# Kernel tuning notes

Hardware: AMD Instinct MI355X
Metric: run time of the kernel (lower is better)

The kernel has to match this reference:

```python
import jax, jax.numpy as jnp
import numpy as np

N_NODES = 200000
N_EDGES = 6400000
N_LAYERS = 3
Z_DIM = 4  # 2*4 + 1 + 3 == 12 == Linear in_features


def setup_inputs() -> dict:
    key = jax.random.key(0)
    ks = jax.random.split(key, 7)
    z = jax.random.normal(ks[0], (N_NODES, Z_DIM), dtype=jnp.float32)
    r = jax.random.uniform(ks[1], (N_EDGES, 1), dtype=jnp.float32)
    r_hat = jax.random.normal(ks[2], (N_EDGES, 3), dtype=jnp.float32)
    # Per-layer Linear(12, 1) weights and biases, stacked over layers.
    W = jax.random.normal(ks[3], (N_LAYERS, 1, 12), dtype=jnp.float32) * (1.0 / np.sqrt(12.0))
    b = jnp.zeros((N_LAYERS, 1), dtype=jnp.float32)
    src = jax.random.randint(ks[4], (N_EDGES,), 0, N_NODES, dtype=jnp.int32)
    dst = jax.random.randint(ks[5], (N_EDGES,), 0, N_NODES, dtype=jnp.int32)
    return {"z": z, "r": r, "r_hat": r_hat, "W": W, "b": b, "src": src, "dst": dst}


def reference(z, r, r_hat, W, b, src, dst):
    # batch['x'] = batch['z'].copy()
    x = z
    n_nodes = z.shape[0]
    for i in range(W.shape[0]):
        # Per-edge gather + concat -> [E, 12]
        inpt = jnp.concatenate([z[src], z[dst], r, r_hat], axis=-1)
        # Tiny Linear(12, 1) -> per-edge scalar message [E, 1]
        msg = inpt @ W[i].T + b[i]
        # Scatter-sum messages onto destination nodes, residual update.
        agg = jax.ops.segment_sum(msg, dst, num_segments=n_nodes)  # [N, 1]
        z = z + agg  # broadcast over the 4 node features
    return z, x
```

## Files before the change

kernel.cpp:

```cpp
#include <hip/hip_runtime.h>

#define N_NODES 200000
#define N_EDGES 6400000
#define K_BUCKETS 256
#define BUCKET 784
#define NSB 3200
#define CHUNK 2000
#define P_SPLIT 8

__device__ __forceinline__ unsigned short f2bf(float x) {
    unsigned u = __float_as_uint(x);
    u += 0x7fffu + ((u >> 16) & 1u);
    return (unsigned short)(u >> 16);
}
__device__ __forceinline__ float bf2f(unsigned short h) {
    return __uint_as_float((unsigned)h << 16);
}


__global__ __launch_bounds__(256) void prep_kernel(
    const float4* __restrict__ z, float4* __restrict__ x_out,
    const float* __restrict__ W,
    float* __restrict__ u, float* __restrict__ v)
{
    int n = blockIdx.x * 256 + threadIdx.x;
    if (n >= N_NODES) return;
    float4 zv = z[n];
    x_out[n] = zv;
    float a0 = W[0], a1 = W[1], a2 = W[2], a3 = W[3];
    float q0 = W[4], q1 = W[5], q2 = W[6], q3 = W[7];
    u[n] = a0 * zv.x + a1 * zv.y + a2 * zv.z + a3 * zv.w;
    v[n] = q0 * zv.x + q1 * zv.y + q2 * zv.z + q3 * zv.w;
}

__global__ __launch_bounds__(256) void hist_kernel(const int* __restrict__ dst,
                                                   int* __restrict__ counts)
{
    __shared__ int cnt[K_BUCKETS];
    int tid = threadIdx.x, sb = blockIdx.x;
    cnt[tid] = 0;
    __syncthreads();
    int e0 = sb * CHUNK;
    for (int i = tid; i < CHUNK; i += 256)
        atomicAdd(&cnt[dst[e0 + i] / BUCKET], 1);
    __syncthreads();
    counts[sb * K_BUCKETS + tid] = cnt[tid];
}

__global__ __launch_bounds__(256) void scan_cols(const int* __restrict__ counts,
                                                 int* __restrict__ baseRel,
                                                 int* __restrict__ tot)
{
    __shared__ int buf[256];
    __shared__ int carry_s;
    int k = blockIdx.x, tid = threadIdx.x;
    if (tid == 0) carry_s = 0;
    __syncthreads();
    for (int base = 0; base < NSB; base += 256) {
        int idx = base + tid;
        int v = (idx < NSB) ? counts[idx * K_BUCKETS + k] : 0;
        buf[tid] = v;
        __syncthreads();
        for (int off = 1; off < 256; off <<= 1) {
            int t = (tid >= off) ? buf[tid - off] : 0;
            __syncthreads();
            buf[tid] += t;
            __syncthreads();
        }
        int incl = buf[tid];
        if (idx < NSB) baseRel[idx * K_BUCKETS + k] = carry_s + incl - v;
        __syncthreads();
        if (tid == 255) carry_s += incl;
        __syncthreads();
    }
    if (tid == 255) tot[k] = carry_s;
}

__global__ __launch_bounds__(256) void scan_tot(const int* __restrict__ tot,
                                                int* __restrict__ bstart)
{
    __shared__ int buf[256];
    int tid = threadIdx.x;
    int v = tot[tid];
    buf[tid] = v;
    __syncthreads();
    for (int off = 1; off < 256; off <<= 1) {
        int t = (tid >= off) ? buf[tid - off] : 0;
        __syncthreads();
        buf[tid] += t;
        __syncthreads();
    }
    bstart[tid] = buf[tid] - v;
    if (tid == 255) bstart[256] = buf[255];
}

__global__ __launch_bounds__(256) void scatter_kernel(
    const int* __restrict__ src, const int* __restrict__ dst,
    const float* __restrict__ r, const float* __restrict__ r_hat,
    const float* __restrict__ W, const float* __restrict__ b,
    const int* __restrict__ counts, const int* __restrict__ baseRel,
    const int* __restrict__ bstart,
    int* __restrict__ packedA, unsigned* __restrict__ c01a,
    unsigned short* __restrict__ c2a)
{
    __shared__ int cur[K_BUCKETS];
    __shared__ int delta[K_BUCKETS];
    __shared__ int scanbuf[256];
    __shared__ int            lpack[CHUNK];
    __shared__ unsigned       lc01[CHUNK];
    __shared__ unsigned short lc2[CHUNK];
    __shared__ unsigned char  skb[CHUNK];

    int tid = threadIdx.x, sb = blockIdx.x;

    int v = counts[sb * K_BUCKETS + tid];
    scanbuf[tid] = v;
    __syncthreads();
    for (int off = 1; off < 256; off <<= 1) {
        int t = (tid >= off) ? scanbuf[tid - off] : 0;
        __syncthreads();
        scanbuf[tid] += t;
        __syncthreads();
    }
    int localBase = scanbuf[tid] - v;
    int gBase = bstart[tid] + baseRel[sb * K_BUCKETS + tid];
    delta[tid] = gBase - localBase;
    cur[tid] = localBase;
    __syncthreads();

    float w8_0 = W[8],  w9_0 = W[9],  w10_0 = W[10], w11_0 = W[11], b0 = b[0];
    float w8_1 = W[20], w9_1 = W[21], w10_1 = W[22], w11_1 = W[23], b1 = b[1];
    float w8_2 = W[32], w9_2 = W[33], w10_2 = W[34], w11_2 = W[35], b2 = b[2];

    int e0 = sb * CHUNK;
    for (int i = tid; i < CHUNK; i += 256) {
        int e = e0 + i;
        int d = dst[e];
        int k = d / BUCKET;
        int dl = d - k * BUCKET;
        int slot = atomicAdd(&cur[k], 1);
        int sn = src[e];
        float rv = r[e];
        size_t he = 3 * (size_t)e;
        float h0 = r_hat[he], h1 = r_hat[he + 1], h2 = r_hat[he + 2];
        lpack[slot] = (sn << 10) | dl;
        unsigned cc0 = f2bf(w8_0 * rv + w9_0 * h0 + w10_0 * h1 + w11_0 * h2 + b0);
        unsigned cc1 = f2bf(w8_1 * rv + w9_1 * h0 + w10_1 * h1 + w11_1 * h2 + b1);
        lc01[slot] = cc0 | (cc1 << 16);
        lc2[slot]  = f2bf(w8_2 * rv + w9_2 * h0 + w10_2 * h1 + w11_2 * h2 + b2);
        skb[slot]  = (unsigned char)k;
    }
    __syncthreads();

    for (int s = tid; s < CHUNK; s += 256) {
        int k = skb[s];
        int gpos = delta[k] + s;
        packedA[gpos] = lpack[s];
        c01a[gpos] = lc01[s];
        c2a[gpos]  = lc2[s];
    }
}

__global__ __launch_bounds__(256) void pagg_kernel(
    const int* __restrict__ packedA, const unsigned* __restrict__ c01a,
    const unsigned short* __restrict__ c2a, const int* __restrict__ bstart,
    const float* __restrict__ u, const float* __restrict__ v,
    int layer, float* __restrict__ partial)
{
    __shared__ float vsl[BUCKET];
    __shared__ float aggsl[BUCKET];
    int tid = threadIdx.x, blk = blockIdx.x;
    int k = blk / P_SPLIT;
    int p = blk - k * P_SPLIT;
    int nbase = k * BUCKET;
    int nn = min(BUCKET, N_NODES - nbase);

    for (int i = tid; i < BUCKET; i += 256) {
        aggsl[i] = 0.0f;
        vsl[i] = (i < nn) ? v[nbase + i] : 0.0f;
    }
    __syncthreads();

    int estart = bstart[k], eend = bstart[k + 1];
    int len = eend - estart;
    int per = (len + P_SPLIT - 1) / P_SPLIT;
    int lo = estart + p * per;
    int hi = min(lo + per, eend);

    for (int j = lo + tid; j < hi; j += 256) {
        int pack = packedA[j];
        int s = pack >> 10;
        int dl = pack & 1023;
        float c = (layer == 2) ? bf2f(c2a[j])
                               : bf2f((unsigned short)(c01a[j] >> (16 * layer)));
        atomicAdd(&aggsl[dl], u[s] + vsl[dl] + c);
    }
    __syncthreads();

    float* pout = partial + (size_t)blk * BUCKET;
    for (int i = tid; i < BUCKET; i += 256) pout[i] = aggsl[i];
}

__global__ __launch_bounds__(256) void fin_kernel(
    const float4* __restrict__ z0, const float* __restrict__ partial,
    const float* __restrict__ Sin, float* __restrict__ Sout,
    const float* __restrict__ W, int layer,
    float* __restrict__ u, float* __restrict__ v, float4* __restrict__ z_out)
{
    int n = blockIdx.x * 256 + threadIdx.x;
    if (n >= N_NODES) return;
    int k = n / BUCKET;
    int i = n - k * BUCKET;
    float agg = 0.0f;
    const float* pk = partial + (size_t)k * P_SPLIT * BUCKET + i;
#pragma unroll
    for (int p = 0; p < P_SPLIT; ++p) agg += pk[(size_t)p * BUCKET];
    float S = ((layer == 0) ? 0.0f : Sin[n]) + agg;
    if (layer < 2) {
        const float* Wn = W + 12 * (layer + 1);
        float a0 = Wn[0], a1 = Wn[1], a2 = Wn[2], a3 = Wn[3];
        float q0 = Wn[4], q1 = Wn[5], q2 = Wn[6], q3 = Wn[7];
        float A = a0 + a1 + a2 + a3, B = q0 + q1 + q2 + q3;
        float4 zv = z0[n];
        Sout[n] = S;
        u[n] = a0 * zv.x + a1 * zv.y + a2 * zv.z + a3 * zv.w + A * S;
        v[n] = q0 * zv.x + q1 * zv.y + q2 * zv.z + q3 * zv.w + B * S;
    } else {
        float4 zv = z0[n];
        zv.x += S; zv.y += S; zv.z += S; zv.w += S;
        z_out[n] = zv;
    }
}


__global__ __launch_bounds__(256) void init_kernel(
    const float4* __restrict__ z_in, float4* __restrict__ z_cur,
    float4* __restrict__ x_out, float* __restrict__ agg)
{
    int n = blockIdx.x * blockDim.x + threadIdx.x;
    if (n < N_NODES) {
        float4 vv = z_in[n];
        z_cur[n] = vv; x_out[n] = vv; agg[n] = 0.0f;
    }
}

__global__ __launch_bounds__(256) void edge_kernel(
    const float* __restrict__ z, const float* __restrict__ r,
    const float* __restrict__ r_hat, const int* __restrict__ src,
    const int* __restrict__ dst, const float* __restrict__ Wl,
    const float* __restrict__ bl, float* __restrict__ agg)
{
    int e = blockIdx.x * blockDim.x + threadIdx.x;
    if (e >= N_EDGES) return;
    float w0 = Wl[0], w1 = Wl[1], w2 = Wl[2], w3 = Wl[3];
    float w4 = Wl[4], w5 = Wl[5], w6 = Wl[6], w7 = Wl[7];
    float w8 = Wl[8], w9 = Wl[9], w10 = Wl[10], w11 = Wl[11];
    float bias = bl[0];
    int s = src[e], d = dst[e];
    float4 zs = ((const float4*)z)[s];
    float4 zd = ((const float4*)z)[d];
    float rv = r[e];
    const float* rh = r_hat + 3 * (size_t)e;
    float msg = w0*zs.x + w1*zs.y + w2*zs.z + w3*zs.w
              + w4*zd.x + w5*zd.y + w6*zd.z + w7*zd.w
              + w8*rv + w9*rh[0] + w10*rh[1] + w11*rh[2] + bias;
    unsafeAtomicAdd(&agg[d], msg);
}

__global__ __launch_bounds__(256) void node_update(float4* __restrict__ z_cur,
                                                   float* __restrict__ agg)
{
    int n = blockIdx.x * blockDim.x + threadIdx.x;
    if (n < N_NODES) {
        float a = agg[n]; float4 vv = z_cur[n];
        vv.x += a; vv.y += a; vv.z += a; vv.w += a;
        z_cur[n] = vv; agg[n] = 0.0f;
    }
}

__global__ __launch_bounds__(256) void final_update(const float4* __restrict__ z_cur,
                                                    const float* __restrict__ agg,
                                                    float4* __restrict__ z_out)
{
    int n = blockIdx.x * blockDim.x + threadIdx.x;
    if (n < N_NODES) {
        float a = agg[n]; float4 vv = z_cur[n];
        vv.x += a; vv.y += a; vv.z += a; vv.w += a;
        z_out[n] = vv;
    }
}


extern "C" void kernel_launch(void* const* d_in, const int* in_sizes, int n_in,
                              void* d_out, int out_size, void* d_ws, size_t ws_size,
                              hipStream_t stream)
{
    const float* z     = (const float*)d_in[0];
    const float* r     = (const float*)d_in[1];
    const float* r_hat = (const float*)d_in[2];
    const float* W     = (const float*)d_in[3];
    const float* b     = (const float*)d_in[4];
    const int*   src   = (const int*)d_in[5];
    const int*   dst   = (const int*)d_in[6];
    float* out = (float*)d_out;

    char* ws = (char*)d_ws;
    size_t off = 0;
    auto alloc = [&](size_t bytes) {
        void* p = ws + off;
        off += (bytes + 15) & ~(size_t)15;
        return p;
    };
    int*            packedA = (int*)alloc((size_t)N_EDGES * 4);
    unsigned*       c01a    = (unsigned*)alloc((size_t)N_EDGES * 4);
    unsigned short* c2a     = (unsigned short*)alloc((size_t)N_EDGES * 2);
    int*            counts  = (int*)alloc((size_t)NSB * K_BUCKETS * 4);
    int*            baseRel = (int*)alloc((size_t)NSB * K_BUCKETS * 4);
    int*            tot     = (int*)alloc((size_t)K_BUCKETS * 4);
    int*            bstart  = (int*)alloc((size_t)(K_BUCKETS + 1) * 4);
    float*          Sa      = (float*)alloc((size_t)N_NODES * 4);
    float*          Sb      = (float*)alloc((size_t)N_NODES * 4);
    float*          ubuf    = (float*)alloc((size_t)N_NODES * 4);
    float*          vbuf    = (float*)alloc((size_t)N_NODES * 4);
    float*          partial = (float*)alloc((size_t)K_BUCKETS * P_SPLIT * BUCKET * 4);
    size_t required = off;

    dim3 nblk((N_NODES + 255) / 256);

    if (ws_size >= required) {
        prep_kernel<<<nblk, 256, 0, stream>>>(
            (const float4*)z, (float4*)(out + 4 * (size_t)N_NODES), W, ubuf, vbuf);
        hist_kernel<<<NSB, 256, 0, stream>>>(dst, counts);
        scan_cols<<<K_BUCKETS, 256, 0, stream>>>(counts, baseRel, tot);
        scan_tot<<<1, 256, 0, stream>>>(tot, bstart);
        scatter_kernel<<<NSB, 256, 0, stream>>>(src, dst, r, r_hat, W, b,
                                                counts, baseRel, bstart,
                                                packedA, c01a, c2a);
        pagg_kernel<<<K_BUCKETS * P_SPLIT, 256, 0, stream>>>(
            packedA, c01a, c2a, bstart, ubuf, vbuf, 0, partial);
        fin_kernel<<<nblk, 256, 0, stream>>>(
            (const float4*)z, partial, Sa, Sa, W, 0, ubuf, vbuf, (float4*)out);
        pagg_kernel<<<K_BUCKETS * P_SPLIT, 256, 0, stream>>>(
            packedA, c01a, c2a, bstart, ubuf, vbuf, 1, partial);
        fin_kernel<<<nblk, 256, 0, stream>>>(
            (const float4*)z, partial, Sa, Sb, W, 1, ubuf, vbuf, (float4*)out);
        pagg_kernel<<<K_BUCKETS * P_SPLIT, 256, 0, stream>>>(
            packedA, c01a, c2a, bstart, ubuf, vbuf, 2, partial);
        fin_kernel<<<nblk, 256, 0, stream>>>(
            (const float4*)z, partial, Sb, Sb, W, 2, ubuf, vbuf, (float4*)out);
    } else {
        float* agg   = (float*)d_ws;
        float* z_cur = agg + N_NODES;
        dim3 eblk((N_EDGES + 255) / 256);
        init_kernel<<<nblk, 256, 0, stream>>>(
            (const float4*)z, (float4*)z_cur,
            (float4*)(out + 4 * (size_t)N_NODES), agg);
        for (int i = 0; i < 3; ++i) {
            edge_kernel<<<eblk, 256, 0, stream>>>(
                z_cur, r, r_hat, src, dst, W + 12 * i, b + i, agg);
            if (i < 2)
                node_update<<<nblk, 256, 0, stream>>>((float4*)z_cur, agg);
            else
                final_update<<<nblk, 256, 0, stream>>>(
                    (const float4*)z_cur, agg, (float4*)out);
        }
    }
}
```

Before: 403.5 us.

## Precompute all-layer z-dependent edge sums in one pass, then run lean SpMV layers

The per-layer edge aggregation is split algebraically. One fused pass over the sorted edges gathers bf16-packed initial node features and accumulates, for all three layers at once, the initial-feature message sums plus in-degree. The two remaining layers then need only a plain SpMV of the running residual S over the edges. This cuts per-edge reads of u, v and the constant arrays in later layers, in exchange for four shared atomics per edge in the first pass, larger float4 partial buffers, and bf16 rounding of z.

```diff
diff --git a/kernel.cpp b/kernel.cpp
--- a/kernel.cpp
+++ b/kernel.cpp
@@ -20,17 +20,15 @@
 
 __global__ __launch_bounds__(256) void prep_kernel(
     const float4* __restrict__ z, float4* __restrict__ x_out,
-    const float* __restrict__ W,
-    float* __restrict__ u, float* __restrict__ v)
+    ushort4* __restrict__ zb)
 {
     int n = blockIdx.x * 256 + threadIdx.x;
     if (n >= N_NODES) return;
     float4 zv = z[n];
     x_out[n] = zv;
-    float a0 = W[0], a1 = W[1], a2 = W[2], a3 = W[3];
-    float q0 = W[4], q1 = W[5], q2 = W[6], q3 = W[7];
-    u[n] = a0 * zv.x + a1 * zv.y + a2 * zv.z + a3 * zv.w;
-    v[n] = q0 * zv.x + q1 * zv.y + q2 * zv.z + q3 * zv.w;
+    ushort4 q;
+    q.x = f2bf(zv.x); q.y = f2bf(zv.y); q.z = f2bf(zv.z); q.w = f2bf(zv.w);
+    zb[n] = q;
 }
 
 __global__ __launch_bounds__(256) void hist_kernel(const int* __restrict__ dst,
@@ -161,25 +159,25 @@
     }
 }
 
-__global__ __launch_bounds__(256) void pagg_kernel(
+__global__ __launch_bounds__(256) void ypass_kernel(
     const int* __restrict__ packedA, const unsigned* __restrict__ c01a,
     const unsigned short* __restrict__ c2a, const int* __restrict__ bstart,
-    const float* __restrict__ u, const float* __restrict__ v,
-    int layer, float* __restrict__ partial)
-{
-    __shared__ float vsl[BUCKET];
-    __shared__ float aggsl[BUCKET];
+    const ushort4* __restrict__ zb, const float* __restrict__ W,
+    float4* __restrict__ gpart)
+{
+    __shared__ float g0sl[BUCKET], g1sl[BUCKET], g2sl[BUCKET], dgsl[BUCKET];
     int tid = threadIdx.x, blk = blockIdx.x;
     int k = blk / P_SPLIT;
     int p = blk - k * P_SPLIT;
-    int nbase = k * BUCKET;
-    int nn = min(BUCKET, N_NODES - nbase);
 
     for (int i = tid; i < BUCKET; i += 256) {
-        aggsl[i] = 0.0f;
-        vsl[i] = (i < nn) ? v[nbase + i] : 0.0f;
-    }
-    __syncthreads();
+        g0sl[i] = 0.f; g1sl[i] = 0.f; g2sl[i] = 0.f; dgsl[i] = 0.f;
+    }
+    __syncthreads();
+
+    float a00 = W[0],  a01 = W[1],  a02 = W[2],  a03 = W[3];
+    float a10 = W[12], a11 = W[13], a12 = W[14], a13 = W[15];
+    float a20 = W[24], a21 = W[25], a22 = W[26], a23 = W[27];
 
     int estart = bstart[k], eend = bstart[k + 1];
     int len = eend - estart;
@@ -191,44 +189,106 @@
         int pack = packedA[j];
         int s = pack >> 10;
         int dl = pack & 1023;
-        float c = (layer == 2) ? bf2f(c2a[j])
-                               : bf2f((unsigned short)(c01a[j] >> (16 * layer)));
-        atomicAdd(&aggsl[dl], u[s] + vsl[dl] + c);
-    }
-    __syncthreads();
-
-    float* pout = partial + (size_t)blk * BUCKET;
-    for (int i = tid; i < BUCKET; i += 256) pout[i] = aggsl[i];
-}
-
-__global__ __launch_bounds__(256) void fin_kernel(
-    const float4* __restrict__ z0, const float* __restrict__ partial,
-    const float* __restrict__ Sin, float* __restrict__ Sout,
-    const float* __restrict__ W, int layer,
-    float* __restrict__ u, float* __restrict__ v, float4* __restrict__ z_out)
+        ushort4 zq = zb[s];
+        float z0v = bf2f(zq.x), z1v = bf2f(zq.y), z2v = bf2f(zq.z), z3v = bf2f(zq.w);
+        unsigned cc = c01a[j];
+        float c0 = bf2f((unsigned short)(cc & 0xffff));
+        float c1 = bf2f((unsigned short)(cc >> 16));
+        float c2 = bf2f(c2a[j]);
+        atomicAdd(&g0sl[dl], a00*z0v + a01*z1v + a02*z2v + a03*z3v + c0);
+        atomicAdd(&g1sl[dl], a10*z0v + a11*z1v + a12*z2v + a13*z3v + c1);
+        atomicAdd(&g2sl[dl], a20*z0v + a21*z1v + a22*z2v + a23*z3v + c2);
+        atomicAdd(&dgsl[dl], 1.0f);
+    }
+    __syncthreads();
+
+    float4* pout = gpart + (size_t)blk * BUCKET;
+    for (int i = tid; i < BUCKET; i += 256) {
+        float4 o; o.x = g0sl[i]; o.y = g1sl[i]; o.z = g2sl[i]; o.w = dgsl[i];
+        pout[i] = o;
+    }
+}
+
+__global__ __launch_bounds__(256) void fin0_kernel(
+    const float4* __restrict__ gpart, const float4* __restrict__ z0,
+    const float* __restrict__ W,
+    float* __restrict__ g1, float* __restrict__ g2, float* __restrict__ deg,
+    float* __restrict__ S1)
 {
     int n = blockIdx.x * 256 + threadIdx.x;
     if (n >= N_NODES) return;
     int k = n / BUCKET;
     int i = n - k * BUCKET;
-    float agg = 0.0f;
+    const float4* pk = gpart + (size_t)k * P_SPLIT * BUCKET + i;
+    float4 acc = pk[0];
+#pragma unroll
+    for (int p = 1; p < P_SPLIT; ++p) {
+        float4 t = pk[(size_t)p * BUCKET];
+        acc.x += t.x; acc.y += t.y; acc.z += t.z; acc.w += t.w;
+    }
+    g1[n] = acc.y; g2[n] = acc.z; deg[n] = acc.w;
+    float q0 = W[4], q1 = W[5], q2 = W[6], q3 = W[7];
+    float4 zv = z0[n];
+    S1[n] = acc.x + acc.w * (q0*zv.x + q1*zv.y + q2*zv.z + q3*zv.w);
+}
+
+__global__ __launch_bounds__(256) void spmv_kernel(
+    const int* __restrict__ packedA, const int* __restrict__ bstart,
+    const float* __restrict__ S, float* __restrict__ partial)
+{
+    __shared__ float tsl[BUCKET];
+    int tid = threadIdx.x, blk = blockIdx.x;
+    int k = blk / P_SPLIT;
+    int p = blk - k * P_SPLIT;
+    for (int i = tid; i < BUCKET; i += 256) tsl[i] = 0.f;
+    __syncthreads();
+
+    int estart = bstart[k], eend = bstart[k + 1];
+    int len = eend - estart;
+    int per = (len + P_SPLIT - 1) / P_SPLIT;
+    int lo = estart + p * per;
+    int hi = min(lo + per, eend);
+
+    for (int j = lo + tid; j < hi; j += 256) {
+        int pack = packedA[j];
+        int s = pack >> 10;
+        int dl = pack & 1023;
+        atomicAdd(&tsl[dl], S[s]);
+    }
+    __syncthreads();
+    float* pout = partial + (size_t)blk * BUCKET;
+    for (int i = tid; i < BUCKET; i += 256) pout[i] = tsl[i];
+}
+
+template<int LAST>
+__global__ __launch_bounds__(256) void finl_kernel(
+    const float* __restrict__ partial, const float* __restrict__ gl,
+    const float* __restrict__ deg, const float4* __restrict__ z0,
+    const float* __restrict__ Sin, float* __restrict__ Sout,
+    const float* __restrict__ W, int layer, float4* __restrict__ z_out)
+{
+    int n = blockIdx.x * 256 + threadIdx.x;
+    if (n >= N_NODES) return;
+    int k = n / BUCKET;
+    int i = n - k * BUCKET;
     const float* pk = partial + (size_t)k * P_SPLIT * BUCKET + i;
+    float t = 0.f;
 #pragma unroll
-    for (int p = 0; p < P_SPLIT; ++p) agg += pk[(size_t)p * BUCKET];
-    float S = ((layer == 0) ? 0.0f : Sin[n]) + agg;
-    if (layer < 2) {
-        const float* Wn = W + 12 * (layer + 1);
-        float a0 = Wn[0], a1 = Wn[1], a2 = Wn[2], a3 = Wn[3];
-        float q0 = Wn[4], q1 = Wn[5], q2 = Wn[6], q3 = Wn[7];
-        float A = a0 + a1 + a2 + a3, B = q0 + q1 + q2 + q3;
-        float4 zv = z0[n];
-        Sout[n] = S;
-        u[n] = a0 * zv.x + a1 * zv.y + a2 * zv.z + a3 * zv.w + A * S;
-        v[n] = q0 * zv.x + q1 * zv.y + q2 * zv.z + q3 * zv.w + B * S;
+    for (int p = 0; p < P_SPLIT; ++p) t += pk[(size_t)p * BUCKET];
+    const float* Wl = W + 12 * layer;
+    float a0 = Wl[0], a1 = Wl[1], a2 = Wl[2], a3 = Wl[3];
+    float q0 = Wl[4], q1 = Wl[5], q2 = Wl[6], q3 = Wl[7];
+    float A = a0 + a1 + a2 + a3, B = q0 + q1 + q2 + q3;
+    float S = Sin[n];
+    float4 zv = z0[n];
+    float agg = gl[n] + A * t + deg[n] * (q0*zv.x + q1*zv.y + q2*zv.z + q3*zv.w + B * S);
+    float Sn = S + agg;
+    if (LAST) {
+        float4 o = zv;
+        o.x += Sn; o.y += Sn; o.z += Sn; o.w += Sn;
+        z_out[n] = o;
     } else {
-        float4 zv = z0[n];
-        zv.x += S; zv.y += S; zv.z += S; zv.w += S;
-        z_out[n] = zv;
+        Sout[n] = Sn;
     }
 }
 
@@ -318,36 +378,37 @@
     int*            baseRel = (int*)alloc((size_t)NSB * K_BUCKETS * 4);
     int*            tot     = (int*)alloc((size_t)K_BUCKETS * 4);
     int*            bstart  = (int*)alloc((size_t)(K_BUCKETS + 1) * 4);
+    ushort4*        zb      = (ushort4*)alloc((size_t)N_NODES * 8);
+    float4*         gpart   = (float4*)alloc((size_t)K_BUCKETS * P_SPLIT * BUCKET * 16);
+    float*          g1      = (float*)alloc((size_t)N_NODES * 4);
+    float*          g2      = (float*)alloc((size_t)N_NODES * 4);
+    float*          deg     = (float*)alloc((size_t)N_NODES * 4);
     float*          Sa      = (float*)alloc((size_t)N_NODES * 4);
     float*          Sb      = (float*)alloc((size_t)N_NODES * 4);
-    float*          ubuf    = (float*)alloc((size_t)N_NODES * 4);
-    float*          vbuf    = (float*)alloc((size_t)N_NODES * 4);
-    float*          partial = (float*)alloc((size_t)K_BUCKETS * P_SPLIT * BUCKET * 4);
+    float*          pspmv   = (float*)alloc((size_t)K_BUCKETS * P_SPLIT * BUCKET * 4);
     size_t required = off;
 
     dim3 nblk((N_NODES + 255) / 256);
 
     if (ws_size >= required) {
         prep_kernel<<<nblk, 256, 0, stream>>>(
-            (const float4*)z, (float4*)(out + 4 * (size_t)N_NODES), W, ubuf, vbuf);
+            (const float4*)z, (float4*)(out + 4 * (size_t)N_NODES), zb);
         hist_kernel<<<NSB, 256, 0, stream>>>(dst, counts);
         scan_cols<<<K_BUCKETS, 256, 0, stream>>>(counts, baseRel, tot);
         scan_tot<<<1, 256, 0, stream>>>(tot, bstart);
         scatter_kernel<<<NSB, 256, 0, stream>>>(src, dst, r, r_hat, W, b,
                                                 counts, baseRel, bstart,
                                                 packedA, c01a, c2a);
-        pagg_kernel<<<K_BUCKETS * P_SPLIT, 256, 0, stream>>>(
-            packedA, c01a, c2a, bstart, ubuf, vbuf, 0, partial);
-        fin_kernel<<<nblk, 256, 0, stream>>>(
-            (const float4*)z, partial, Sa, Sa, W, 0, ubuf, vbuf, (float4*)out);
-        pagg_kernel<<<K_BUCKETS * P_SPLIT, 256, 0, stream>>>(
-            packedA, c01a, c2a, bstart, ubuf, vbuf, 1, partial);
-        fin_kernel<<<nblk, 256, 0, stream>>>(
-            (const float4*)z, partial, Sa, Sb, W, 1, ubuf, vbuf, (float4*)out);
-        pagg_kernel<<<K_BUCKETS * P_SPLIT, 256, 0, stream>>>(
-            packedA, c01a, c2a, bstart, ubuf, vbuf, 2, partial);
-        fin_kernel<<<nblk, 256, 0, stream>>>(
-            (const float4*)z, partial, Sb, Sb, W, 2, ubuf, vbuf, (float4*)out);
+        ypass_kernel<<<K_BUCKETS * P_SPLIT, 256, 0, stream>>>(
+            packedA, c01a, c2a, bstart, zb, W, gpart);
+        fin0_kernel<<<nblk, 256, 0, stream>>>(
+            gpart, (const float4*)z, W, g1, g2, deg, Sa);
+        spmv_kernel<<<K_BUCKETS * P_SPLIT, 256, 0, stream>>>(packedA, bstart, Sa, pspmv);
+        finl_kernel<0><<<nblk, 256, 0, stream>>>(
+            pspmv, g1, deg, (const float4*)z, Sa, Sb, W, 1, (float4*)out);
+        spmv_kernel<<<K_BUCKETS * P_SPLIT, 256, 0, stream>>>(packedA, bstart, Sb, pspmv);
+        finl_kernel<1><<<nblk, 256, 0, stream>>>(
+            pspmv, g2, deg, (const float4*)z, Sb, Sa, W, 2, (float4*)out);
     } else {
         float* agg   = (float*)d_ws;
         float* z_cur = agg + N_NODES;
```

New measurement: 495.4 us. 22.8% more time.

## Factor destination term out of edge aggregation using in-degree and split bf16 coefficient arrays

Applied to the files above, without the earlier changes.

The per-edge dst-node term v[dst] is pulled out of the scatter loop and applied once per node as degree times v, with in-degree counted in the first aggregation pass. The edge pass now reads one gathered src-node table and one compact bf16 coefficient array per layer, where before it loaded a packed 32-bit pair. The aggregation, scatter and histogram loops are also unrolled, with int4 loads for dst, to raise memory-level parallelism. The trade-off is an extra shared-memory atomic and partial buffer in the first pass and a per-node degree array.

```diff
diff --git a/kernel.cpp b/kernel.cpp
--- a/kernel.cpp
+++ b/kernel.cpp
@@ -20,17 +20,13 @@
 
 __global__ __launch_bounds__(256) void prep_kernel(
     const float4* __restrict__ z, float4* __restrict__ x_out,
-    const float* __restrict__ W,
-    float* __restrict__ u, float* __restrict__ v)
+    const float* __restrict__ W, float* __restrict__ wtab)
 {
     int n = blockIdx.x * 256 + threadIdx.x;
     if (n >= N_NODES) return;
     float4 zv = z[n];
     x_out[n] = zv;
-    float a0 = W[0], a1 = W[1], a2 = W[2], a3 = W[3];
-    float q0 = W[4], q1 = W[5], q2 = W[6], q3 = W[7];
-    u[n] = a0 * zv.x + a1 * zv.y + a2 * zv.z + a3 * zv.w;
-    v[n] = q0 * zv.x + q1 * zv.y + q2 * zv.z + q3 * zv.w;
+    wtab[n] = W[0]*zv.x + W[1]*zv.y + W[2]*zv.z + W[3]*zv.w;
 }
 
 __global__ __launch_bounds__(256) void hist_kernel(const int* __restrict__ dst,
@@ -41,8 +37,14 @@
     cnt[tid] = 0;
     __syncthreads();
     int e0 = sb * CHUNK;
-    for (int i = tid; i < CHUNK; i += 256)
-        atomicAdd(&cnt[dst[e0 + i] / BUCKET], 1);
+    const int4* d4p = (const int4*)(dst + e0);
+    for (int i4 = tid; i4 < CHUNK / 4; i4 += 256) {
+        int4 d4 = d4p[i4];
+        atomicAdd(&cnt[d4.x / BUCKET], 1);
+        atomicAdd(&cnt[d4.y / BUCKET], 1);
+        atomicAdd(&cnt[d4.z / BUCKET], 1);
+        atomicAdd(&cnt[d4.w / BUCKET], 1);
+    }
     __syncthreads();
     counts[sb * K_BUCKETS + tid] = cnt[tid];
 }
@@ -100,14 +102,16 @@
     const float* __restrict__ W, const float* __restrict__ b,
     const int* __restrict__ counts, const int* __restrict__ baseRel,
     const int* __restrict__ bstart,
-    int* __restrict__ packedA, unsigned* __restrict__ c01a,
+    int* __restrict__ packedA,
+    unsigned short* __restrict__ c0a, unsigned short* __restrict__ c1a,
     unsigned short* __restrict__ c2a)
 {
     __shared__ int cur[K_BUCKETS];
     __shared__ int delta[K_BUCKETS];
     __shared__ int scanbuf[256];
     __shared__ int            lpack[CHUNK];
-    __shared__ unsigned       lc01[CHUNK];
+    __shared__ unsigned short lc0[CHUNK];
+    __shared__ unsigned short lc1[CHUNK];
     __shared__ unsigned short lc2[CHUNK];
     __shared__ unsigned char  skb[CHUNK];
 
@@ -133,7 +137,33 @@
     float w8_2 = W[32], w9_2 = W[33], w10_2 = W[34], w11_2 = W[35], b2 = b[2];
 
     int e0 = sb * CHUNK;
-    for (int i = tid; i < CHUNK; i += 256) {
+    int i = tid;
+    for (; i + 256 < CHUNK; i += 512) {
+        int ea = e0 + i, eb = e0 + i + 256;
+        int da = dst[ea], db = dst[eb];
+        int sa = src[ea], sb2 = src[eb];
+        float ra = r[ea], rb = r[eb];
+        size_t ha = 3 * (size_t)ea, hb = 3 * (size_t)eb;
+        float a0h = r_hat[ha], a1h = r_hat[ha+1], a2h = r_hat[ha+2];
+        float b0h = r_hat[hb], b1h = r_hat[hb+1], b2h = r_hat[hb+2];
+
+        int ka = da / BUCKET, dla = da - ka * BUCKET;
+        int slota = atomicAdd(&cur[ka], 1);
+        lpack[slota] = (sa << 10) | dla;
+        lc0[slota] = f2bf(w8_0*ra + w9_0*a0h + w10_0*a1h + w11_0*a2h + b0);
+        lc1[slota] = f2bf(w8_1*ra + w9_1*a0h + w10_1*a1h + w11_1*a2h + b1);
+        lc2[slota] = f2bf(w8_2*ra + w9_2*a0h + w10_2*a1h + w11_2*a2h + b2);
+        skb[slota] = (unsigned char)ka;
+
+        int kb = db / BUCKET, dlb = db - kb * BUCKET;
+        int slotb = atomicAdd(&cur[kb], 1);
+        lpack[slotb] = (sb2 << 10) | dlb;
+        lc0[slotb] = f2bf(w8_0*rb + w9_0*b0h + w10_0*b1h + w11_0*b2h + b0);
+        lc1[slotb] = f2bf(w8_1*rb + w9_1*b0h + w10_1*b1h + w11_1*b2h + b1);
+        lc2[slotb] = f2bf(w8_2*rb + w9_2*b0h + w10_2*b1h + w11_2*b2h + b2);
+        skb[slotb] = (unsigned char)kb;
+    }
+    for (; i < CHUNK; i += 256) {
         int e = e0 + i;
         int d = dst[e];
         int k = d / BUCKET;
@@ -142,13 +172,12 @@
         int sn = src[e];
         float rv = r[e];
         size_t he = 3 * (size_t)e;
-        float h0 = r_hat[he], h1 = r_hat[he + 1], h2 = r_hat[he + 2];
+        float h0 = r_hat[he], h1 = r_hat[he+1], h2 = r_hat[he+2];
         lpack[slot] = (sn << 10) | dl;
-        unsigned cc0 = f2bf(w8_0 * rv + w9_0 * h0 + w10_0 * h1 + w11_0 * h2 + b0);
-        unsigned cc1 = f2bf(w8_1 * rv + w9_1 * h0 + w10_1 * h1 + w11_1 * h2 + b1);
-        lc01[slot] = cc0 | (cc1 << 16);
-        lc2[slot]  = f2bf(w8_2 * rv + w9_2 * h0 + w10_2 * h1 + w11_2 * h2 + b2);
-        skb[slot]  = (unsigned char)k;
+        lc0[slot] = f2bf(w8_0*rv + w9_0*h0 + w10_0*h1 + w11_0*h2 + b0);
+        lc1[slot] = f2bf(w8_1*rv + w9_1*h0 + w10_1*h1 + w11_1*h2 + b1);
+        lc2[slot] = f2bf(w8_2*rv + w9_2*h0 + w10_2*h1 + w11_2*h2 + b2);
+        skb[slot] = (unsigned char)k;
     }
     __syncthreads();
 
@@ -156,28 +185,27 @@
         int k = skb[s];
         int gpos = delta[k] + s;
         packedA[gpos] = lpack[s];
-        c01a[gpos] = lc01[s];
-        c2a[gpos]  = lc2[s];
-    }
-}
-
-__global__ __launch_bounds__(256) void pagg_kernel(
-    const int* __restrict__ packedA, const unsigned* __restrict__ c01a,
-    const unsigned short* __restrict__ c2a, const int* __restrict__ bstart,
-    const float* __restrict__ u, const float* __restrict__ v,
-    int layer, float* __restrict__ partial)
-{
-    __shared__ float vsl[BUCKET];
-    __shared__ float aggsl[BUCKET];
+        c0a[gpos] = lc0[s];
+        c1a[gpos] = lc1[s];
+        c2a[gpos] = lc2[s];
+    }
+}
+
+template<int FIRST>
+__global__ __launch_bounds__(256) void gpass_kernel(
+    const int* __restrict__ packedA, const unsigned short* __restrict__ cb,
+    const int* __restrict__ bstart, const float* __restrict__ wtab,
+    float* __restrict__ gpart, float* __restrict__ dpart)
+{
+    __shared__ float gsl[BUCKET];
+    __shared__ float dsl[FIRST ? BUCKET : 1];
     int tid = threadIdx.x, blk = blockIdx.x;
     int k = blk / P_SPLIT;
     int p = blk - k * P_SPLIT;
-    int nbase = k * BUCKET;
-    int nn = min(BUCKET, N_NODES - nbase);
 
     for (int i = tid; i < BUCKET; i += 256) {
-        aggsl[i] = 0.0f;
-        vsl[i] = (i < nn) ? v[nbase + i] : 0.0f;
+        gsl[i] = 0.0f;
+        if (FIRST) dsl[i] = 0.0f;
     }
     __syncthreads();
 
@@ -187,48 +215,86 @@
     int lo = estart + p * per;
     int hi = min(lo + per, eend);
 
-    for (int j = lo + tid; j < hi; j += 256) {
-        int pack = packedA[j];
-        int s = pack >> 10;
-        int dl = pack & 1023;
-        float c = (layer == 2) ? bf2f(c2a[j])
-                               : bf2f((unsigned short)(c01a[j] >> (16 * layer)));
-        atomicAdd(&aggsl[dl], u[s] + vsl[dl] + c);
-    }
-    __syncthreads();
-
-    float* pout = partial + (size_t)blk * BUCKET;
-    for (int i = tid; i < BUCKET; i += 256) pout[i] = aggsl[i];
+    int j = lo + tid;
+    for (; j + 768 < hi; j += 1024) {
+        int p0 = packedA[j];
+        int p1 = packedA[j + 256];
+        int p2 = packedA[j + 512];
+        int p3 = packedA[j + 768];
+        unsigned short q0 = cb[j], q1 = cb[j + 256], q2 = cb[j + 512], q3 = cb[j + 768];
+        float g0 = wtab[p0 >> 10];
+        float g1 = wtab[p1 >> 10];
+        float g2 = wtab[p2 >> 10];
+        float g3 = wtab[p3 >> 10];
+        atomicAdd(&gsl[p0 & 1023], g0 + bf2f(q0));
+        atomicAdd(&gsl[p1 & 1023], g1 + bf2f(q1));
+        atomicAdd(&gsl[p2 & 1023], g2 + bf2f(q2));
+        atomicAdd(&gsl[p3 & 1023], g3 + bf2f(q3));
+        if (FIRST) {
+            atomicAdd(&dsl[p0 & 1023], 1.0f);
+            atomicAdd(&dsl[p1 & 1023], 1.0f);
+            atomicAdd(&dsl[p2 & 1023], 1.0f);
+            atomicAdd(&dsl[p3 & 1023], 1.0f);
+        }
+    }
+    for (; j < hi; j += 256) {
+        int pk = packedA[j];
+        atomicAdd(&gsl[pk & 1023], wtab[pk >> 10] + bf2f(cb[j]));
+        if (FIRST) atomicAdd(&dsl[pk & 1023], 1.0f);
+    }
+    __syncthreads();
+
+    float* gout = gpart + (size_t)blk * BUCKET;
+    for (int i = tid; i < BUCKET; i += 256) {
+        gout[i] = gsl[i];
+        if (FIRST) dpart[(size_t)blk * BUCKET + i] = dsl[i];
+    }
 }
 
 __global__ __launch_bounds__(256) void fin_kernel(
-    const float4* __restrict__ z0, const float* __restrict__ partial,
-    const float* __restrict__ Sin, float* __restrict__ Sout,
-    const float* __restrict__ W, int layer,
-    float* __restrict__ u, float* __restrict__ v, float4* __restrict__ z_out)
+    const float* __restrict__ gpart, const float* __restrict__ dpart,
+    const float4* __restrict__ z0, const float* __restrict__ Sin,
+    float* __restrict__ Sout, float* __restrict__ deg,
+    const float* __restrict__ W, int layer, float* __restrict__ wnext,
+    float4* __restrict__ z_out)
 {
     int n = blockIdx.x * 256 + threadIdx.x;
     if (n >= N_NODES) return;
     int k = n / BUCKET;
     int i = n - k * BUCKET;
-    float agg = 0.0f;
-    const float* pk = partial + (size_t)k * P_SPLIT * BUCKET + i;
+    const float* gk = gpart + (size_t)k * P_SPLIT * BUCKET + i;
+    float G = 0.0f;
 #pragma unroll
-    for (int p = 0; p < P_SPLIT; ++p) agg += pk[(size_t)p * BUCKET];
-    float S = ((layer == 0) ? 0.0f : Sin[n]) + agg;
+    for (int p = 0; p < P_SPLIT; ++p) G += gk[(size_t)p * BUCKET];
+
+    float dg;
+    if (layer == 0) {
+        const float* dk = dpart + (size_t)k * P_SPLIT * BUCKET + i;
+        dg = 0.0f;
+#pragma unroll
+        for (int p = 0; p < P_SPLIT; ++p) dg += dk[(size_t)p * BUCKET];
+        deg[n] = dg;
+    } else {
+        dg = deg[n];
+    }
+
+    const float* Wl = W + 12 * layer;
+    float q0 = Wl[4], q1 = Wl[5], q2 = Wl[6], q3 = Wl[7];
+    float B = q0 + q1 + q2 + q3;
+    float4 zv = z0[n];
+    float S = (layer == 0) ? 0.0f : Sin[n];
+    float Sn = S + G + dg * (q0*zv.x + q1*zv.y + q2*zv.z + q3*zv.w + B * S);
+
     if (layer < 2) {
+        Sout[n] = Sn;
         const float* Wn = W + 12 * (layer + 1);
         float a0 = Wn[0], a1 = Wn[1], a2 = Wn[2], a3 = Wn[3];
-        float q0 = Wn[4], q1 = Wn[5], q2 = Wn[6], q3 = Wn[7];
-        float A = a0 + a1 + a2 + a3, B = q0 + q1 + q2 + q3;
-        float4 zv = z0[n];
-        Sout[n] = S;
-        u[n] = a0 * zv.x + a1 * zv.y + a2 * zv.z + a3 * zv.w + A * S;
-        v[n] = q0 * zv.x + q1 * zv.y + q2 * zv.z + q3 * zv.w + B * S;
+        float A = a0 + a1 + a2 + a3;
+        wnext[n] = a0*zv.x + a1*zv.y + a2*zv.z + a3*zv.w + A * Sn;
     } else {
-        float4 zv = z0[n];
-        zv.x += S; zv.y += S; zv.z += S; zv.w += S;
-        z_out[n] = zv;
+        float4 o = zv;
+        o.x += Sn; o.y += Sn; o.z += Sn; o.w += Sn;
+        z_out[n] = o;
     }
 }
 
@@ -312,42 +378,44 @@
         return p;
     };
     int*            packedA = (int*)alloc((size_t)N_EDGES * 4);
-    unsigned*       c01a    = (unsigned*)alloc((size_t)N_EDGES * 4);
+    unsigned short* c0a     = (unsigned short*)alloc((size_t)N_EDGES * 2);
+    unsigned short* c1a     = (unsigned short*)alloc((size_t)N_EDGES * 2);
     unsigned short* c2a     = (unsigned short*)alloc((size_t)N_EDGES * 2);
     int*            counts  = (int*)alloc((size_t)NSB * K_BUCKETS * 4);
     int*            baseRel = (int*)alloc((size_t)NSB * K_BUCKETS * 4);
     int*            tot     = (int*)alloc((size_t)K_BUCKETS * 4);
     int*            bstart  = (int*)alloc((size_t)(K_BUCKETS + 1) * 4);
+    float*          wtab    = (float*)alloc((size_t)N_NODES * 4);
     float*          Sa      = (float*)alloc((size_t)N_NODES * 4);
     float*          Sb      = (float*)alloc((size_t)N_NODES * 4);
-    float*          ubuf    = (float*)alloc((size_t)N_NODES * 4);
-    float*          vbuf    = (float*)alloc((size_t)N_NODES * 4);
-    float*          partial = (float*)alloc((size_t)K_BUCKETS * P_SPLIT * BUCKET * 4);
+    float*          deg     = (float*)alloc((size_t)N_NODES * 4);
+    float*          gpart   = (float*)alloc((size_t)K_BUCKETS * P_SPLIT * BUCKET * 4);
+    float*          dpart   = (float*)alloc((size_t)K_BUCKETS * P_SPLIT * BUCKET * 4);
     size_t required = off;
 
     dim3 nblk((N_NODES + 255) / 256);
 
     if (ws_size >= required) {
         prep_kernel<<<nblk, 256, 0, stream>>>(
-            (const float4*)z, (float4*)(out + 4 * (size_t)N_NODES), W, ubuf, vbuf);
+            (const float4*)z, (float4*)(out + 4 * (size_t)N_NODES), W, wtab);
         hist_kernel<<<NSB, 256, 0, stream>>>(dst, counts);
         scan_cols<<<K_BUCKETS, 256, 0, stream>>>(counts, baseRel, tot);
         scan_tot<<<1, 256, 0, stream>>>(tot, bstart);
         scatter_kernel<<<NSB, 256, 0, stream>>>(src, dst, r, r_hat, W, b,
                                                 counts, baseRel, bstart,
-                                                packedA, c01a, c2a);
-        pagg_kernel<<<K_BUCKETS * P_SPLIT, 256, 0, stream>>>(
-            packedA, c01a, c2a, bstart, ubuf, vbuf, 0, partial);
+                                                packedA, c0a, c1a, c2a);
+        gpass_kernel<1><<<K_BUCKETS * P_SPLIT, 256, 0, stream>>>(
+            packedA, c0a, bstart, wtab, gpart, dpart);
         fin_kernel<<<nblk, 256, 0, stream>>>(
-            (const float4*)z, partial, Sa, Sa, W, 0, ubuf, vbuf, (float4*)out);
-        pagg_kernel<<<K_BUCKETS * P_SPLIT, 256, 0, stream>>>(
-            packedA, c01a, c2a, bstart, ubuf, vbuf, 1, partial);
+            gpart, dpart, (const float4*)z, Sa, Sa, deg, W, 0, wtab, (float4*)out);
+        gpass_kernel<0><<<K_BUCKETS * P_SPLIT, 256, 0, stream>>>(
+            packedA, c1a, bstart, wtab, gpart, dpart);
         fin_kernel<<<nblk, 256, 0, stream>>>(
-            (const float4*)z, partial, Sa, Sb, W, 1, ubuf, vbuf, (float4*)out);
-        pagg_kernel<<<K_BUCKETS * P_SPLIT, 256, 0, stream>>>(
-            packedA, c01a, c2a, bstart, ubuf, vbuf, 2, partial);
+            gpart, dpart, (const float4*)z, Sa, Sb, deg, W, 1, wtab, (float4*)out);
+        gpass_kernel<0><<<K_BUCKETS * P_SPLIT, 256, 0, stream>>>(
+            packedA, c2a, bstart, wtab, gpart, dpart);
         fin_kernel<<<nblk, 256, 0, stream>>>(
-            (const float4*)z, partial, Sb, Sb, W, 2, ubuf, vbuf, (float4*)out);
+            gpart, dpart, (const float4*)z, Sb, Sa, deg, W, 2, wtab, (float4*)out);
     } else {
         float* agg   = (float*)d_ws;
         float* z_cur = agg + N_NODES;
```

New measurement: 430.4 us. +6.7%, slower.
